# Optimization experiments

Measured on AMD Instinct MI355X. Metric: run time of the kernel, lower is better.

The kernel has to match this reference:

```python
import jax, jax.numpy as jnp
import numpy as np

C = 64
K = 3  # kernel_size
B, H, W = 8, 128, 128


def conv2d(x, w, b, pad, groups=1):
    y = jax.lax.conv_general_dilated(
        x, w, window_strides=(1, 1), padding=[(pad, pad), (pad, pad)],
        feature_group_count=groups, dimension_numbers=('NCHW', 'OIHW', 'NCHW'))
    return y + b[None, :, None, None]


def setup_inputs() -> dict:
    key = jax.random.key(0)
    ks = jax.random.split(key, 11)
    s3 = 1.0 / np.sqrt(C * 9)  # kaiming-ish scale for 3x3 convs
    inp = {
        'x':  jax.random.normal(ks[0], (B, C, H, W), jnp.float32),
        'w0': jax.random.normal(ks[1], (C, C, 3, 3), jnp.float32) * s3,
        'b0': jax.random.normal(ks[2], (C,), jnp.float32) * 0.01,
        'w1': jax.random.normal(ks[3], (C, 1, 3, 3), jnp.float32) * (1.0 / 3.0),  # depthwise
        'b1': jax.random.normal(ks[4], (C,), jnp.float32) * 0.01,
        'w2': jax.random.normal(ks[5], (1, 1, K), jnp.float32) * (1.0 / np.sqrt(K)),  # conv1d over channel axis
        'b2': jax.random.normal(ks[6], (1,), jnp.float32) * 0.01,
        'w3': jax.random.normal(ks[7], (C * K * K, C, 1, 1), jnp.float32) * (1.0 / np.sqrt(C)),  # 1x1 -> dynamic filters
        'b3': jax.random.normal(ks[8], (C * K * K,), jnp.float32) * 0.01,
        'wf': jax.random.normal(ks[9], (C, C, 3, 3), jnp.float32) * s3,
        'bf': jax.random.normal(ks[10], (C,), jnp.float32) * 0.01,
    }
    return inp


def reference(x, w0, b0, w1, b1, w2, b2, w3, b3, wf, bf):
    b, c, h, w = x.shape
    pre = x
    # conv0: dense 3x3
    x0 = conv2d(x, w0, b0, pad=1)
    # conv1: depthwise 3x3
    x1 = conv2d(x0, w1, b1, pad=1, groups=c)
    # ECA-style channel attention: global avg pool -> conv1d over channel dim
    m = jnp.mean(x0, axis=(2, 3))  # [b, c]
    x2 = jax.lax.conv_general_dilated(
        m[:, None, :], w2, window_strides=(1,), padding=[(K // 2, K // 2)],
        dimension_numbers=('NCH', 'OIH', 'NCH')) + b2[None, :, None]  # [b, 1, c]
    out = x1 + x2[:, 0, :, None, None]  # broadcast [b,c,1,1] over h,w
    # conv3: 1x1 producing per-pixel dynamic filters [b, c*9, h, w]
    fil = jnp.einsum('oc,bchw->bohw', w3[:, :, 0, 0], out) + b3[None, :, None, None]
    filter_x = fil.reshape(b, c, K * K, h, w)
    # unfold(x0): 3x3 patches, channel-major then row-major kernel positions
    xp = jnp.pad(x0, ((0, 0), (0, 0), (1, 1), (1, 1)))
    unfold_x = jnp.stack(
        [xp[:, :, i:i + h, j:j + w] for i in range(3) for j in range(3)], axis=2)  # [b,c,9,h,w]
    out = jnp.sum(unfold_x * filter_x, axis=2)  # per-pixel dynamic conv
    out = jnp.where(out >= 0, out, 0.2 * out)  # LeakyReLU(0.2)
    out = conv2d(out, wf, bf, pad=1) + pre
    return out
```

## Files before the change

kernel.cpp:

```cpp
#include <hip/hip_runtime.h>

#define BB 8
#define C 64
#define HH 128
#define WW 128
#define HW (HH*WW)

#define TS 72
#define NPX 324
#define NCALL 41

typedef __attribute__((ext_vector_type(8))) short short8;
typedef __attribute__((ext_vector_type(4))) unsigned short us4;
typedef __attribute__((ext_vector_type(4))) float f32x4;

__device__ inline unsigned short f2bf(float f) {
    union { float f; unsigned u; } v; v.f = f;
    unsigned r = v.u + 0x7fff + ((v.u >> 16) & 1);
    return (unsigned short)(r >> 16);
}
__device__ inline float bf2f(unsigned short h) {
    union { unsigned u; float f; } v; v.u = ((unsigned)h) << 16;
    return v.f;
}

__device__ __forceinline__ void gload16(const void* g, void* l) {
    __builtin_amdgcn_global_load_lds(
        (const __attribute__((address_space(1))) void*)g,
        (__attribute__((address_space(3))) void*)l, 16, 0, 0);
}

__device__ __forceinline__ void stage_tile_nhwc(
    const unsigned short* __restrict__ in, unsigned short* tile,
    const unsigned short* __restrict__ zpad,
    const int b, const int h0, const int w0, const int t)
{
    const int wv = t >> 6, ln = t & 63;
    const int pxo = ln >> 3, s = ln & 7;
    for (int call = wv; call < NCALL; call += 4) {
        const int px = call*8 + pxo;
        const int o  = s ^ (px & 7);
        const int th = px / 18, tw = px - th*18;
        const int gh = h0 + th - 1, gw = w0 + tw - 1;
        const unsigned short* src = zpad;
        if (px < NPX && (unsigned)gh < HH && (unsigned)gw < WW)
            src = &in[((size_t)(b*HW) + gh*WW + gw)*C + o*8];
        gload16(src, &tile[call*8*64]);
    }
}

__global__ __launch_bounds__(256) void prep_kernel(
    const float* __restrict__ w0, const float* __restrict__ wf,
    const float* __restrict__ w3, const float* __restrict__ b3,
    unsigned short* __restrict__ wb0, unsigned short* __restrict__ wbf,
    unsigned short* __restrict__ wb3, float* __restrict__ b3r,
    float* __restrict__ m, unsigned short* __restrict__ zpad)
{
    const int t = blockIdx.x * 256 + threadIdx.x;
    for (int i = t; i < C*C*9; i += 128*256) {
        int p = i % 9; int rest = i / 9; int ci = rest % C; int oc = rest / C;
        wb0[(p*C + oc)*C + ci] = f2bf(w0[i]);
        wbf[(p*C + oc)*C + ci] = f2bf(wf[i]);
    }
    for (int i = t; i < 9*C*C; i += 128*256) {
        int j = i >> 12, oc = (i >> 6) & 63, k = i & 63;
        wb3[i] = f2bf(w3[(oc*9 + j)*C + k]);
    }
    for (int i = t; i < 9*C; i += 128*256) {
        int j = i >> 6, oc = i & 63;
        b3r[i] = b3[oc*9 + j];
    }
    for (int i = t; i < BB*C; i += 128*256) m[i] = 0.f;
    if (t < 128) zpad[t] = 0;
}

__global__ __launch_bounds__(256) void conv0_kernel(
    const float* __restrict__ in,
    const unsigned short* __restrict__ wb,
    const float* __restrict__ bias,
    unsigned short* __restrict__ outp,
    float* __restrict__ m)
{
    __shared__ __align__(16) unsigned short tile[NPX*TS];
    __shared__ __align__(16) float sred[4][4][16];
    const int b  = blockIdx.z;
    const int h0 = blockIdx.y * 16;
    const int w0 = blockIdx.x * 16;
    const int t  = threadIdx.x;

    {
        const int pxi = t & 31, g = t >> 5;
        for (int px = pxi; px < NPX; px += 32) {
            int th = px / 18, tw = px - th*18;
            int gh = h0 + th - 1, gw = w0 + tw - 1;
            short8 v = {0,0,0,0,0,0,0,0};
            if ((unsigned)gh < HH && (unsigned)gw < WW) {
                const float* sp = in + ((size_t)(b*C + g*8)*HW + gh*WW + gw);
#pragma unroll
                for (int k = 0; k < 8; ++k) v[k] = (short)f2bf(sp[k*HW]);
            }
            *(short8*)&tile[px*TS + g*8] = v;
        }
    }
    __syncthreads();

    const int wid = t >> 6, ln = t & 63;
    const int l15 = ln & 15, q = ln >> 4;

    f32x4 acc[4][4];
#pragma unroll
    for (int mg = 0; mg < 4; ++mg)
#pragma unroll
        for (int nt = 0; nt < 4; ++nt) acc[mg][nt] = (f32x4){0.f,0.f,0.f,0.f};

#pragma unroll
    for (int p = 0; p < 9; ++p) {
        const int dh = p / 3, dw = p % 3;
#pragma unroll
        for (int ks = 0; ks < 2; ++ks) {
            short8 bfrag[4];
#pragma unroll
            for (int nt = 0; nt < 4; ++nt)
                bfrag[nt] = *(const short8*)&wb[((size_t)(p*C) + nt*16 + l15)*C + ks*32 + q*8];
            short8 afrag[4];
#pragma unroll
            for (int mg = 0; mg < 4; ++mg) {
                const int r = wid*4 + mg;
                afrag[mg] = *(const short8*)&tile[((r+dh)*18 + l15 + dw)*TS + ks*32 + q*8];
            }
#pragma unroll
            for (int mg = 0; mg < 4; ++mg)
#pragma unroll
                for (int nt = 0; nt < 4; ++nt)
                    acc[mg][nt] = __builtin_amdgcn_mfma_f32_16x16x32_bf16(
                        afrag[mg], bfrag[nt], acc[mg][nt], 0, 0, 0);
        }
    }

    unsigned short* x0o = outp;
#pragma unroll
    for (int nt = 0; nt < 4; ++nt) {
        const int oc = nt*16 + l15;
        const float bv = bias[oc];
        float s = 0.f;
#pragma unroll
        for (int mg = 0; mg < 4; ++mg) {
            const int hh = h0 + wid*4 + mg;
#pragma unroll
            for (int reg = 0; reg < 4; ++reg) {
                const int wwp = w0 + q*4 + reg;
                const unsigned short sv = f2bf(acc[mg][nt][reg] + bv);
                x0o[((size_t)(b*HW) + hh*WW + wwp)*C + oc] = sv;
                s += bf2f(sv);
            }
        }
        s += __shfl_xor(s, 16);
        s += __shfl_xor(s, 32);
        if (q == 0) sred[wid][nt][l15] = s;
    }
    __syncthreads();
    if (t < 64) {
        float s = sred[0][t >> 4][t & 15] + sred[1][t >> 4][t & 15]
                + sred[2][t >> 4][t & 15] + sred[3][t >> 4][t & 15];
        atomicAdd(&m[b*C + t], s * (1.f/(float)HW));
    }
}

__global__ __launch_bounds__(256) void convf_kernel(
    const unsigned short* __restrict__ in,
    const unsigned short* __restrict__ wb,
    const float* __restrict__ bias,
    const float* __restrict__ res,
    float* __restrict__ outg,
    const unsigned short* __restrict__ zpad)
{
    __shared__ __align__(16) unsigned short tile[NCALL*8*64];
    const int b  = blockIdx.z;
    const int h0 = blockIdx.y * 16;
    const int w0 = blockIdx.x * 16;
    const int t  = threadIdx.x;

    stage_tile_nhwc(in, tile, zpad, b, h0, w0, t);
    __syncthreads();

    const int wid = t >> 6, ln = t & 63;
    const int l15 = ln & 15, q = ln >> 4;

    f32x4 acc[4][4];
#pragma unroll
    for (int mg = 0; mg < 4; ++mg)
#pragma unroll
        for (int nt = 0; nt < 4; ++nt) acc[mg][nt] = (f32x4){0.f,0.f,0.f,0.f};

#pragma unroll
    for (int p = 0; p < 9; ++p) {
        const int dh = p / 3, dw = p % 3;
#pragma unroll
        for (int ks = 0; ks < 2; ++ks) {
            short8 bfrag[4];
#pragma unroll
            for (int nt = 0; nt < 4; ++nt)
                bfrag[nt] = *(const short8*)&wb[((size_t)(p*C) + nt*16 + l15)*C + ks*32 + q*8];
            short8 afrag[4];
#pragma unroll
            for (int mg = 0; mg < 4; ++mg) {
                const int px = (wid*4 + mg + dh)*18 + l15 + dw;
                const int o  = (ks*4 + q) ^ (px & 7);
                afrag[mg] = *(const short8*)&tile[px*64 + o*8];
            }
#pragma unroll
            for (int mg = 0; mg < 4; ++mg)
#pragma unroll
                for (int nt = 0; nt < 4; ++nt)
                    acc[mg][nt] = __builtin_amdgcn_mfma_f32_16x16x32_bf16(
                        bfrag[nt], afrag[mg], acc[mg][nt], 0, 0, 0);
        }
    }

#pragma unroll
    for (int mg = 0; mg < 4; ++mg) {
        const int hh = h0 + wid*4 + mg;
#pragma unroll
        for (int nt = 0; nt < 4; ++nt) {
            const f32x4 bv4 = *(const f32x4*)&bias[nt*16 + q*4];
#pragma unroll
            for (int reg = 0; reg < 4; ++reg) {
                const int oc = nt*16 + q*4 + reg;
                const size_t base = (size_t)(b*C + oc)*HW + hh*WW + w0 + l15;
                outg[base] = acc[mg][nt][reg] + bv4[reg] + res[base];
            }
        }
    }
}

__global__ __launch_bounds__(256) void fused_kernel(
    const unsigned short* __restrict__ x0,
    const float* __restrict__ w1, const float* __restrict__ b1,
    const float* __restrict__ w2, const float* __restrict__ b2,
    const unsigned short* __restrict__ wb3,
    const float* __restrict__ b3r,
    const float* __restrict__ m,
    unsigned short* __restrict__ y,
    const unsigned short* __restrict__ zpad)
{
    __shared__ __align__(16) unsigned short tile[NCALL*8*64];
    __shared__ __align__(16) unsigned short alds[256*64];
    __shared__ __align__(16) float att[64];
    const int b  = blockIdx.z;
    const int h0 = blockIdx.y * 16;
    const int w0 = blockIdx.x * 16;
    const int t  = threadIdx.x;

    if (t < 64) {
        const float mc = m[b*C + t];
        const float mp = (t > 0)  ? m[b*C + t - 1] : 0.f;
        const float mn = (t < 63) ? m[b*C + t + 1] : 0.f;
        att[t] = b1[t] + fmaf(w2[0], mp, fmaf(w2[1], mc, fmaf(w2[2], mn, b2[0])));
    }
    stage_tile_nhwc(x0, tile, zpad, b, h0, w0, t);
    __syncthreads();

    const int r = t >> 4, cc = t & 15;

    float outv[64];
#pragma unroll
    for (int g = 0; g < 8; ++g) {
        float dw8[8];
#pragma unroll
        for (int k = 0; k < 8; ++k) dw8[k] = 0.f;
#pragma unroll
        for (int j = 0; j < 9; ++j) {
            const int px = (r + j/3)*18 + cc + (j%3);
            const short8 v = *(const short8*)&tile[px*64 + ((g ^ (px&7))*8)];
#pragma unroll
            for (int k = 0; k < 8; ++k)
                dw8[k] = fmaf(w1[(g*8+k)*9 + j], bf2f((unsigned short)v[k]), dw8[k]);
        }
#pragma unroll
        for (int k = 0; k < 8; ++k)
            outv[g*8 + k] = dw8[k] + att[g*8 + k];
    }

    {
        const int sw = t & 7;
#pragma unroll
        for (int g = 0; g < 8; ++g) {
            short8 v;
#pragma unroll
            for (int k = 0; k < 8; ++k) v[k] = (short)f2bf(outv[g*8 + k]);
            *(short8*)&alds[t*64 + ((g ^ sw) * 8)] = v;
        }
    }
    __syncthreads();

    const int wid = t >> 6, ln = t & 63;
    const int l15 = ln & 15, q = ln >> 4;

    short8 afrag[4][2];
#pragma unroll
    for (int mg = 0; mg < 4; ++mg) {
        const int px = (wid*4 + mg)*16 + l15;
        const int sw = px & 7;
#pragma unroll
        for (int ks = 0; ks < 2; ++ks)
            afrag[mg][ks] = *(const short8*)&alds[px*64 + (((ks*4 + q) ^ sw) * 8)];
    }

    f32x4 y_acc[4][4];
#pragma unroll
    for (int mg = 0; mg < 4; ++mg)
#pragma unroll
        for (int nt = 0; nt < 4; ++nt) y_acc[mg][nt] = (f32x4){0.f,0.f,0.f,0.f};

#pragma unroll 1
    for (int j = 0; j < 9; ++j) {
        const int dh = j / 3, dw = j - dh*3;
#pragma unroll
        for (int ntoc = 0; ntoc < 4; ++ntoc) {
            const short8 bf0 = *(const short8*)&wb3[((size_t)(j*64 + ntoc*16 + l15))*64 + q*8];
            const short8 bf1 = *(const short8*)&wb3[((size_t)(j*64 + ntoc*16 + l15))*64 + 32 + q*8];
            const f32x4 b3v4 = *(const f32x4*)&b3r[j*64 + ntoc*16 + q*4];
#pragma unroll
            for (int mg = 0; mg < 4; ++mg) {
                f32x4 a = b3v4;
                a = __builtin_amdgcn_mfma_f32_16x16x32_bf16(bf0, afrag[mg][0], a, 0, 0, 0);
                a = __builtin_amdgcn_mfma_f32_16x16x32_bf16(bf1, afrag[mg][1], a, 0, 0, 0);
                const int px = (wid*4 + mg + dh)*18 + l15 + dw;
                const int o  = (ntoc*2 + (q >> 1)) ^ (px & 7);
                const us4 pv = *(const us4*)&tile[px*64 + o*8 + (q & 1)*4];
#pragma unroll
                for (int reg = 0; reg < 4; ++reg)
                    y_acc[mg][ntoc][reg] = fmaf(a[reg], bf2f(pv[reg]), y_acc[mg][ntoc][reg]);
            }
        }
    }

    __syncthreads();
    unsigned short* ybuf = alds;
#pragma unroll
    for (int mg = 0; mg < 4; ++mg) {
        const int rr = wid*4 + mg;
        const int px = rr*16 + l15;
        const int swy = (px & 7) << 1;
#pragma unroll
        for (int ntoc = 0; ntoc < 4; ++ntoc) {
            us4 ov;
#pragma unroll
            for (int reg = 0; reg < 4; ++reg) {
                float v = y_acc[mg][ntoc][reg];
                v = (v >= 0.f) ? v : 0.2f * v;
                ov[reg] = f2bf(v);
            }
            const int slot = (ntoc*4 + q) ^ swy;
            *(us4*)&ybuf[px*64 + slot*4] = ov;
        }
    }
    __syncthreads();
    for (int id = t; id < 2048; id += 256) {
        int px = id >> 3, g = id & 7;
        const int swy = (px & 7) << 1;
        short8 v = *(const short8*)&ybuf[px*64 + ((2*g) ^ swy)*4];
        int rr = px >> 4, cw = px & 15;
        *(short8*)&y[((size_t)(b*HW) + (h0+rr)*WW + (w0+cw))*C + g*8] = v;
    }
}

extern "C" void kernel_launch(void* const* d_in, const int* in_sizes, int n_in,
                              void* d_out, int out_size, void* d_ws, size_t ws_size,
                              hipStream_t stream) {
    const float* x  = (const float*)d_in[0];
    const float* w0 = (const float*)d_in[1];
    const float* b0 = (const float*)d_in[2];
    const float* w1 = (const float*)d_in[3];
    const float* b1 = (const float*)d_in[4];
    const float* w2 = (const float*)d_in[5];
    const float* b2 = (const float*)d_in[6];
    const float* w3 = (const float*)d_in[7];
    const float* b3 = (const float*)d_in[8];
    const float* wf = (const float*)d_in[9];
    const float* bf = (const float*)d_in[10];
    float* out = (float*)d_out;

    unsigned short* x0  = (unsigned short*)d_ws;
    unsigned short* y   = x0 + (size_t)BB*HW*C;
    float*          m   = (float*)(y + (size_t)BB*HW*C);
    unsigned short* wb0 = (unsigned short*)(m + BB*C);
    unsigned short* wbf = wb0 + 9*C*C;
    unsigned short* wb3 = wbf + 9*C*C;
    float*          b3r = (float*)(wb3 + 9*C*C);
    unsigned short* zpad = (unsigned short*)(b3r + 9*C);

    prep_kernel<<<128, 256, 0, stream>>>(w0, wf, w3, b3, wb0, wbf, wb3, b3r, m, zpad);
    conv0_kernel<<<dim3(8,8,8), 256, 0, stream>>>(x, wb0, b0, x0, m);
    fused_kernel<<<dim3(8,8,8), 256, 0, stream>>>(x0, w1, b1, w2, b2, wb3, b3r, m, y, zpad);
    convf_kernel<<<dim3(8,8,8), 256, 0, stream>>>(y, wbf, bf, x, out, zpad);
}
```

Baseline: 212.2 us.

## Double block size to 512 threads and split work across eight waves

All three main kernels now launch 512 threads per block. In the two dense convolutions each wave covers half the output channels and four rows, and in the fused kernel each wave covers two rows. The depthwise stage is reassigned so that two threads share one pixel, each handling half the channel groups. The aim is more waves per block to hide latency with the same 512-block grid, since 512 blocks is only about two per CU. The trade-off is more redundant A-fragment LDS reads in the convs and different register pressure under launch_bounds(512,2).

```diff
diff --git a/kernel.cpp b/kernel.cpp
--- a/kernel.cpp
+++ b/kernel.cpp
@@ -30,14 +30,14 @@
         (__attribute__((address_space(3))) void*)l, 16, 0, 0);
 }
 
-__device__ __forceinline__ void stage_tile_nhwc(
+__device__ __forceinline__ void stage_tile_nhwc8(
     const unsigned short* __restrict__ in, unsigned short* tile,
     const unsigned short* __restrict__ zpad,
     const int b, const int h0, const int w0, const int t)
 {
     const int wv = t >> 6, ln = t & 63;
     const int pxo = ln >> 3, s = ln & 7;
-    for (int call = wv; call < NCALL; call += 4) {
+    for (int call = wv; call < NCALL; call += 8) {
         const int px = call*8 + pxo;
         const int o  = s ^ (px & 7);
         const int th = px / 18, tw = px - th*18;
@@ -74,7 +74,7 @@
     if (t < 128) zpad[t] = 0;
 }
 
-__global__ __launch_bounds__(256) void conv0_kernel(
+__global__ __launch_bounds__(512, 2) void conv0_kernel(
     const float* __restrict__ in,
     const unsigned short* __restrict__ wb,
     const float* __restrict__ bias,
@@ -82,15 +82,15 @@
     float* __restrict__ m)
 {
     __shared__ __align__(16) unsigned short tile[NPX*TS];
-    __shared__ __align__(16) float sred[4][4][16];
+    __shared__ __align__(16) float sred[2][2][4][16];
     const int b  = blockIdx.z;
     const int h0 = blockIdx.y * 16;
     const int w0 = blockIdx.x * 16;
     const int t  = threadIdx.x;
 
     {
-        const int pxi = t & 31, g = t >> 5;
-        for (int px = pxi; px < NPX; px += 32) {
+        const int pxi = t & 63, g = t >> 6;
+        for (int px = pxi; px < NPX; px += 64) {
             int th = px / 18, tw = px - th*18;
             int gh = h0 + th - 1, gw = w0 + tw - 1;
             short8 v = {0,0,0,0,0,0,0,0};
@@ -106,32 +106,31 @@
 
     const int wid = t >> 6, ln = t & 63;
     const int l15 = ln & 15, q = ln >> 4;
-
-    f32x4 acc[4][4];
+    const int ng = wid & 1, wr = wid >> 1;
+
+    f32x4 acc[4][2];
 #pragma unroll
     for (int mg = 0; mg < 4; ++mg)
 #pragma unroll
-        for (int nt = 0; nt < 4; ++nt) acc[mg][nt] = (f32x4){0.f,0.f,0.f,0.f};
+        for (int nt = 0; nt < 2; ++nt) acc[mg][nt] = (f32x4){0.f,0.f,0.f,0.f};
 
 #pragma unroll
     for (int p = 0; p < 9; ++p) {
         const int dh = p / 3, dw = p % 3;
 #pragma unroll
         for (int ks = 0; ks < 2; ++ks) {
-            short8 bfrag[4];
-#pragma unroll
-            for (int nt = 0; nt < 4; ++nt)
-                bfrag[nt] = *(const short8*)&wb[((size_t)(p*C) + nt*16 + l15)*C + ks*32 + q*8];
+            short8 bfrag[2];
+#pragma unroll
+            for (int nt = 0; nt < 2; ++nt)
+                bfrag[nt] = *(const short8*)&wb[((size_t)(p*C) + ng*32 + nt*16 + l15)*C + ks*32 + q*8];
             short8 afrag[4];
 #pragma unroll
-            for (int mg = 0; mg < 4; ++mg) {
-                const int r = wid*4 + mg;
-                afrag[mg] = *(const short8*)&tile[((r+dh)*18 + l15 + dw)*TS + ks*32 + q*8];
-            }
-#pragma unroll
             for (int mg = 0; mg < 4; ++mg)
-#pragma unroll
-                for (int nt = 0; nt < 4; ++nt)
+                afrag[mg] = *(const short8*)&tile[((wr*4 + mg + dh)*18 + l15 + dw)*TS + ks*32 + q*8];
+#pragma unroll
+            for (int mg = 0; mg < 4; ++mg)
+#pragma unroll
+                for (int nt = 0; nt < 2; ++nt)
                     acc[mg][nt] = __builtin_amdgcn_mfma_f32_16x16x32_bf16(
                         afrag[mg], bfrag[nt], acc[mg][nt], 0, 0, 0);
         }
@@ -139,13 +138,13 @@
 
     unsigned short* x0o = outp;
 #pragma unroll
-    for (int nt = 0; nt < 4; ++nt) {
-        const int oc = nt*16 + l15;
+    for (int nt = 0; nt < 2; ++nt) {
+        const int oc = ng*32 + nt*16 + l15;
         const float bv = bias[oc];
         float s = 0.f;
 #pragma unroll
         for (int mg = 0; mg < 4; ++mg) {
-            const int hh = h0 + wid*4 + mg;
+            const int hh = h0 + wr*4 + mg;
 #pragma unroll
             for (int reg = 0; reg < 4; ++reg) {
                 const int wwp = w0 + q*4 + reg;
@@ -156,17 +155,18 @@
         }
         s += __shfl_xor(s, 16);
         s += __shfl_xor(s, 32);
-        if (q == 0) sred[wid][nt][l15] = s;
+        if (q == 0) sred[ng][nt][wr][l15] = s;
     }
     __syncthreads();
     if (t < 64) {
-        float s = sred[0][t >> 4][t & 15] + sred[1][t >> 4][t & 15]
-                + sred[2][t >> 4][t & 15] + sred[3][t >> 4][t & 15];
+        const int g2 = t >> 5, nt2 = (t >> 4) & 1, l2 = t & 15;
+        float s = sred[g2][nt2][0][l2] + sred[g2][nt2][1][l2]
+                + sred[g2][nt2][2][l2] + sred[g2][nt2][3][l2];
         atomicAdd(&m[b*C + t], s * (1.f/(float)HW));
     }
 }
 
-__global__ __launch_bounds__(256) void convf_kernel(
+__global__ __launch_bounds__(512, 2) void convf_kernel(
     const unsigned short* __restrict__ in,
     const unsigned short* __restrict__ wb,
     const float* __restrict__ bias,
@@ -180,38 +180,39 @@
     const int w0 = blockIdx.x * 16;
     const int t  = threadIdx.x;
 
-    stage_tile_nhwc(in, tile, zpad, b, h0, w0, t);
+    stage_tile_nhwc8(in, tile, zpad, b, h0, w0, t);
     __syncthreads();
 
     const int wid = t >> 6, ln = t & 63;
     const int l15 = ln & 15, q = ln >> 4;
-
-    f32x4 acc[4][4];
+    const int ng = wid & 1, wr = wid >> 1;
+
+    f32x4 acc[4][2];
 #pragma unroll
     for (int mg = 0; mg < 4; ++mg)
 #pragma unroll
-        for (int nt = 0; nt < 4; ++nt) acc[mg][nt] = (f32x4){0.f,0.f,0.f,0.f};
+        for (int nt = 0; nt < 2; ++nt) acc[mg][nt] = (f32x4){0.f,0.f,0.f,0.f};
 
 #pragma unroll
     for (int p = 0; p < 9; ++p) {
         const int dh = p / 3, dw = p % 3;
 #pragma unroll
         for (int ks = 0; ks < 2; ++ks) {
-            short8 bfrag[4];
-#pragma unroll
-            for (int nt = 0; nt < 4; ++nt)
-                bfrag[nt] = *(const short8*)&wb[((size_t)(p*C) + nt*16 + l15)*C + ks*32 + q*8];
+            short8 bfrag[2];
+#pragma unroll
+            for (int nt = 0; nt < 2; ++nt)
+                bfrag[nt] = *(const short8*)&wb[((size_t)(p*C) + ng*32 + nt*16 + l15)*C + ks*32 + q*8];
             short8 afrag[4];
 #pragma unroll
             for (int mg = 0; mg < 4; ++mg) {
-                const int px = (wid*4 + mg + dh)*18 + l15 + dw;
+                const int px = (wr*4 + mg + dh)*18 + l15 + dw;
                 const int o  = (ks*4 + q) ^ (px & 7);
                 afrag[mg] = *(const short8*)&tile[px*64 + o*8];
             }
 #pragma unroll
             for (int mg = 0; mg < 4; ++mg)
 #pragma unroll
-                for (int nt = 0; nt < 4; ++nt)
+                for (int nt = 0; nt < 2; ++nt)
                     acc[mg][nt] = __builtin_amdgcn_mfma_f32_16x16x32_bf16(
                         bfrag[nt], afrag[mg], acc[mg][nt], 0, 0, 0);
         }
@@ -219,13 +220,13 @@
 
 #pragma unroll
     for (int mg = 0; mg < 4; ++mg) {
-        const int hh = h0 + wid*4 + mg;
-#pragma unroll
-        for (int nt = 0; nt < 4; ++nt) {
-            const f32x4 bv4 = *(const f32x4*)&bias[nt*16 + q*4];
+        const int hh = h0 + wr*4 + mg;
+#pragma unroll
+        for (int nt = 0; nt < 2; ++nt) {
+            const f32x4 bv4 = *(const f32x4*)&bias[ng*32 + nt*16 + q*4];
 #pragma unroll
             for (int reg = 0; reg < 4; ++reg) {
-                const int oc = nt*16 + q*4 + reg;
+                const int oc = ng*32 + nt*16 + q*4 + reg;
                 const size_t base = (size_t)(b*C + oc)*HW + hh*WW + w0 + l15;
                 outg[base] = acc[mg][nt][reg] + bv4[reg] + res[base];
             }
@@ -233,7 +234,7 @@
     }
 }
 
-__global__ __launch_bounds__(256) void fused_kernel(
+__global__ __launch_bounds__(512, 2) void fused_kernel(
     const unsigned short* __restrict__ x0,
     const float* __restrict__ w1, const float* __restrict__ b1,
     const float* __restrict__ w2, const float* __restrict__ b2,
@@ -257,38 +258,33 @@
         const float mn = (t < 63) ? m[b*C + t + 1] : 0.f;
         att[t] = b1[t] + fmaf(w2[0], mp, fmaf(w2[1], mc, fmaf(w2[2], mn, b2[0])));
     }
-    stage_tile_nhwc(x0, tile, zpad, b, h0, w0, t);
-    __syncthreads();
-
-    const int r = t >> 4, cc = t & 15;
-
-    float outv[64];
-#pragma unroll
-    for (int g = 0; g < 8; ++g) {
-        float dw8[8];
-#pragma unroll
-        for (int k = 0; k < 8; ++k) dw8[k] = 0.f;
-#pragma unroll
-        for (int j = 0; j < 9; ++j) {
-            const int px = (r + j/3)*18 + cc + (j%3);
-            const short8 v = *(const short8*)&tile[px*64 + ((g ^ (px&7))*8)];
+    stage_tile_nhwc8(x0, tile, zpad, b, h0, w0, t);
+    __syncthreads();
+
+    {
+        const int px1 = t >> 1, chalf = t & 1;
+        const int r1 = px1 >> 4, c1 = px1 & 15;
+        const int sw1 = px1 & 7;
+#pragma unroll
+        for (int g = 0; g < 4; ++g) {
+            const int kg = chalf*4 + g;
+            float dw8[8];
+#pragma unroll
+            for (int k = 0; k < 8; ++k) dw8[k] = 0.f;
+#pragma unroll
+            for (int j = 0; j < 9; ++j) {
+                const int px = (r1 + j/3)*18 + c1 + (j%3);
+                const short8 v = *(const short8*)&tile[px*64 + ((kg ^ (px&7))*8)];
+#pragma unroll
+                for (int k = 0; k < 8; ++k)
+                    dw8[k] = fmaf(w1[(kg*8 + k)*9 + j],
+                                  bf2f((unsigned short)v[k]), dw8[k]);
+            }
+            short8 ov;
 #pragma unroll
             for (int k = 0; k < 8; ++k)
-                dw8[k] = fmaf(w1[(g*8+k)*9 + j], bf2f((unsigned short)v[k]), dw8[k]);
-        }
-#pragma unroll
-        for (int k = 0; k < 8; ++k)
-            outv[g*8 + k] = dw8[k] + att[g*8 + k];
-    }
-
-    {
-        const int sw = t & 7;
-#pragma unroll
-        for (int g = 0; g < 8; ++g) {
-            short8 v;
-#pragma unroll
-            for (int k = 0; k < 8; ++k) v[k] = (short)f2bf(outv[g*8 + k]);
-            *(short8*)&alds[t*64 + ((g ^ sw) * 8)] = v;
+                ov[k] = (short)f2bf(dw8[k] + att[kg*8 + k]);
+            *(short8*)&alds[px1*64 + ((kg ^ sw1) * 8)] = ov;
         }
     }
     __syncthreads();
@@ -296,19 +292,19 @@
     const int wid = t >> 6, ln = t & 63;
     const int l15 = ln & 15, q = ln >> 4;
 
-    short8 afrag[4][2];
-#pragma unroll
-    for (int mg = 0; mg < 4; ++mg) {
-        const int px = (wid*4 + mg)*16 + l15;
+    short8 afrag[2][2];
+#pragma unroll
+    for (int mg = 0; mg < 2; ++mg) {
+        const int px = (wid*2 + mg)*16 + l15;
         const int sw = px & 7;
 #pragma unroll
         for (int ks = 0; ks < 2; ++ks)
             afrag[mg][ks] = *(const short8*)&alds[px*64 + (((ks*4 + q) ^ sw) * 8)];
     }
 
-    f32x4 y_acc[4][4];
-#pragma unroll
-    for (int mg = 0; mg < 4; ++mg)
+    f32x4 y_acc[2][4];
+#pragma unroll
+    for (int mg = 0; mg < 2; ++mg)
 #pragma unroll
         for (int nt = 0; nt < 4; ++nt) y_acc[mg][nt] = (f32x4){0.f,0.f,0.f,0.f};
 
@@ -321,11 +317,11 @@
             const short8 bf1 = *(const short8*)&wb3[((size_t)(j*64 + ntoc*16 + l15))*64 + 32 + q*8];
             const f32x4 b3v4 = *(const f32x4*)&b3r[j*64 + ntoc*16 + q*4];
 #pragma unroll
-            for (int mg = 0; mg < 4; ++mg) {
+            for (int mg = 0; mg < 2; ++mg) {
                 f32x4 a = b3v4;
                 a = __builtin_amdgcn_mfma_f32_16x16x32_bf16(bf0, afrag[mg][0], a, 0, 0, 0);
                 a = __builtin_amdgcn_mfma_f32_16x16x32_bf16(bf1, afrag[mg][1], a, 0, 0, 0);
-                const int px = (wid*4 + mg + dh)*18 + l15 + dw;
+                const int px = (wid*2 + mg + dh)*18 + l15 + dw;
                 const int o  = (ntoc*2 + (q >> 1)) ^ (px & 7);
                 const us4 pv = *(const us4*)&tile[px*64 + o*8 + (q & 1)*4];
 #pragma unroll
@@ -338,8 +334,8 @@
     __syncthreads();
     unsigned short* ybuf = alds;
 #pragma unroll
-    for (int mg = 0; mg < 4; ++mg) {
-        const int rr = wid*4 + mg;
+    for (int mg = 0; mg < 2; ++mg) {
+        const int rr = wid*2 + mg;
         const int px = rr*16 + l15;
         const int swy = (px & 7) << 1;
 #pragma unroll
@@ -356,7 +352,7 @@
         }
     }
     __syncthreads();
-    for (int id = t; id < 2048; id += 256) {
+    for (int id = t; id < 2048; id += 512) {
         int px = id >> 3, g = id & 7;
         const int swy = (px & 7) << 1;
         short8 v = *(const short8*)&ybuf[px*64 + ((2*g) ^ swy)*4];
@@ -391,7 +387,7 @@
     unsigned short* zpad = (unsigned short*)(b3r + 9*C);
 
     prep_kernel<<<128, 256, 0, stream>>>(w0, wf, w3, b3, wb0, wbf, wb3, b3r, m, zpad);
-    conv0_kernel<<<dim3(8,8,8), 256, 0, stream>>>(x, wb0, b0, x0, m);
-    fused_kernel<<<dim3(8,8,8), 256, 0, stream>>>(x0, w1, b1, w2, b2, wb3, b3r, m, y, zpad);
-    convf_kernel<<<dim3(8,8,8), 256, 0, stream>>>(y, wbf, bf, x, out, zpad);
-}
+    conv0_kernel<<<dim3(8,8,8), 512, 0, stream>>>(x, wb0, b0, x0, m);
+    fused_kernel<<<dim3(8,8,8), 512, 0, stream>>>(x0, w1, b1, w2, b2, wb3, b3r, m, y, zpad);
+    convf_kernel<<<dim3(8,8,8), 512, 0, stream>>>(y, wbf, bf, x, out, zpad);
+}
```

Result: slower. 224.8 us (+6.0%).
